# Kernel tuning notes

Measured on AMD Instinct MI355X. Metric: run time of the kernel, lower is better.

Reference implementation:

```python
import jax, jax.numpy as jnp
import numpy as np

N_QUBITS = 10
N_LAYERS = 2
QSVT_DEGREE = 3
DT_RANK = 5  # n_qubits // 2
PI = np.float32(np.pi)

# ---- batched statevector simulation helpers (wire 0 = most significant, as in pennylane default.qubit) ----

def _apply_1q(s, wire, U):
    # s: (batch,) + (2,)*n complex; U: (batch,2,2) or (2,2)
    s = jnp.moveaxis(s, 1 + wire, 1)
    shp = s.shape
    s2 = s.reshape(shp[0], 2, -1)
    if U.ndim == 3:
        out = jnp.einsum('bij,bjr->bir', U, s2)
    else:
        out = jnp.einsum('ij,bjr->bir', U, s2)
    return jnp.moveaxis(out.reshape(shp), 1, 1 + wire)

def _ry(t):
    c = jnp.cos(t / 2).astype(jnp.complex64)
    s = jnp.sin(t / 2).astype(jnp.complex64)
    return jnp.stack([jnp.stack([c, -s], -1), jnp.stack([s, c], -1)], -2)

def _rz(t):
    e = jnp.exp(-0.5j * jnp.asarray(t).astype(jnp.complex64))
    z = jnp.zeros_like(e)
    return jnp.stack([jnp.stack([e, z], -1), jnp.stack([z, jnp.conj(e)], -1)], -2)

def _rx(t):
    c = jnp.cos(t / 2).astype(jnp.complex64)
    s = (-1j) * jnp.sin(t / 2).astype(jnp.complex64)
    return jnp.stack([jnp.stack([c, s], -1), jnp.stack([s, c], -1)], -2)

def _cnot(s, control, target):
    f = jnp.flip(s, axis=1 + target)
    s0 = jax.lax.index_in_dim(s, 0, axis=1 + control, keepdims=True)
    f1 = jax.lax.index_in_dim(f, 1, axis=1 + control, keepdims=True)
    return jnp.concatenate([s0, f1], axis=1 + control)

def _circuit(h, x, dt, cp, pc):
    """Batched selective QSVT circuit; h,x,dt: (B,n). Returns <Z_i> per wire, (B,n) float32."""
    n = N_QUBITS
    b = h.shape[0]
    s = jnp.zeros((b, 2 ** n), jnp.complex64).at[:, 0].set(1.0).reshape((b,) + (2,) * n)
    # 1. state encoding
    for i in range(n):
        s = _apply_1q(s, i, _ry(h[:, i]))
    # 2. delta-modulated QSVT block
    for d in range(QSVT_DEGREE + 1):
        for i in range(n):
            s = _apply_1q(s, i, _rz(pc[d] * dt[:, i] * PI))
        for i in range(n - 1):
            s = _cnot(s, i, i + 1)
        s = _cnot(s, n - 1, 0)
    # 3. variational block
    k = 0
    for _ in range(N_LAYERS):
        for i in range(n):
            s = _apply_1q(s, i, _rx(cp[k]))
            s = _apply_1q(s, i, _ry(cp[k + 1]))
            s = _apply_1q(s, i, _rz(cp[k + 2]))
            k += 3
        for i in range(n - 1):
            s = _cnot(s, i, i + 1)
    # 4. delta-modulated input encoding
    for i in range(n):
        s = _apply_1q(s, i, _ry(x[:, i] * dt[:, i]))
    # 5. <Z_i> measurements
    p = s.real ** 2 + s.imag ** 2
    zs = [(jax.lax.index_in_dim(p, 0, 1 + i, False) - jax.lax.index_in_dim(p, 1, 1 + i, False)).reshape(b, -1).sum(-1) for i in range(n)]
    return jnp.stack(zs, -1).astype(jnp.float32)

def setup_inputs() -> dict:
    key = jax.random.key(0)
    ks = jax.random.split(key, 6)
    B, S, n, r = 128, 512, N_QUBITS, DT_RANK
    angles = jax.random.uniform(ks[0], (B, S, n), jnp.float32) * PI  # angle encoding in [0, pi]
    W_x = jax.random.normal(ks[1], (r + 2 * n, n), jnp.float32) * 0.3  # x_proj weight (no bias)
    W_dt = jax.random.normal(ks[2], (n, r), jnp.float32) * 0.3  # dt_proj weight
    rng = np.random.default_rng(0)
    dt0 = np.exp(rng.random(n) * (np.log(0.1) - np.log(0.001)) + np.log(0.001))
    b_dt = jnp.asarray(dt0 + np.log(-np.expm1(-dt0)), jnp.float32)  # inverse-softplus init
    poly_coeffs = jax.random.normal(ks[3], (QSVT_DEGREE + 1,), jnp.float32) * 0.1
    circuit_params = jax.random.normal(ks[4], (n * N_LAYERS * 3,), jnp.float32) * 0.1
    D = jnp.ones((n,), jnp.float32)
    return {"angles": angles, "W_x": W_x, "W_dt": W_dt, "b_dt": b_dt,
            "poly_coeffs": poly_coeffs, "circuit_params": circuit_params, "D": D}

def reference(angles, W_x, W_dt, b_dt, poly_coeffs, circuit_params, D):
    # selective projections
    x_dbc = jnp.einsum('bsn,kn->bsk', angles, W_x)
    dt_raw = x_dbc[..., :DT_RANK]
    # B slice (x_dbc[..., DT_RANK:DT_RANK+n]) is computed but unused in the original forward
    C = x_dbc[..., DT_RANK + N_QUBITS:]
    dt = jax.nn.softplus(jnp.einsum('bsr,nr->bsn', dt_raw, W_dt) + b_dt)
    dt_angles = jnp.tanh(dt) * PI
    # quantum recurrence uses detached tensors in the original (torch .detach())
    x_sg = jax.lax.stop_gradient(angles)
    dt_sg = jax.lax.stop_gradient(dt_angles)
    cp = jax.lax.stop_gradient(circuit_params)
    pc = jax.lax.stop_gradient(poly_coeffs)

    def step(h, xs):
        x_t, d_t = xs
        h2 = _circuit(h, x_t, d_t, cp, pc)
        return h2, h2

    h0 = jnp.zeros((angles.shape[0], N_QUBITS), jnp.float32)
    _, hs = jax.lax.scan(step, h0, (jnp.swapaxes(x_sg, 0, 1), jnp.swapaxes(dt_sg, 0, 1)))
    hs = jnp.swapaxes(hs, 0, 1)  # (B,S,n)
    return C * hs + D * angles
```

## Files before the change

### kernel.cpp

```cpp
#include <hip/hip_runtime.h>
#include <math.h>


#define PIF 3.14159265358979323846f

constexpr int NQ = 10, SEQ = 512, NB = 128, NTHR = 512;

struct CTbl { int mz[4][NQ]; };
constexpr CTbl build_tbl() {
  CTbl t{};
  unsigned mrow[NQ];
  for (int b = 0; b < NQ; ++b) mrow[b] = 1u << b;
  for (int d = 0; d < 4; ++d) {
    for (int i = 0; i < NQ; ++i) t.mz[d][i] = (int)mrow[9 - i];
    for (int i = 0; i < NQ - 1; ++i) { int bc = 9 - i, bt = 8 - i; mrow[bt] ^= mrow[bc]; }
    mrow[9] ^= mrow[0];
  }
  return t;
}
constexpr CTbl CT = build_tbl();

struct PermCols { int c4[10]; int cL[10]; };
constexpr PermCols build_perms() {
  PermCols P{};
  for (int b = 0; b < 10; ++b) {
    int x = 1 << b;
    for (int d = 0; d < 4; ++d) {
      for (int i = 0; i < 9; ++i) { int bc = 9 - i, bt = 8 - i; if ((x >> bc) & 1) x ^= (1 << bt); }
      if (x & 1) x ^= (1 << 9);
    }
    P.c4[b] = x;
    int y = 1 << b;
    for (int i = 0; i < 9; ++i) { int bc = 9 - i, bt = 8 - i; if ((y >> bc) & 1) y ^= (1 << bt); }
    P.cL[b] = y;
  }
  return P;
}
constexpr PermCols PC = build_perms();

constexpr int lanePart(int x)  { return ((x >> 0) & 1) | (((x >> 5) & 1) << 1) |
                                        (((x >> 1) & 1) << 2) | (((x >> 7) & 1) << 3) |
                                        (((x >> 3) & 1) << 4) | (((x >> 9) & 1) << 5); }
constexpr int wavePart8(int x) { return ((x >> 4) & 1) | (((x >> 8) & 1) << 1) |
                                        (((x >> 6) & 1) << 2); }

constexpr int kmap(int x) {
  return ((x >> 2) & 1)
       | (((x >> 0) & 1) << 1) | (((x >> 5) & 1) << 2) | (((x >> 1) & 1) << 3)
       | (((x >> 7) & 1) << 4) | (((x >> 3) & 1) << 5) | (((x >> 9) & 1) << 6)
       | (((x >> 4) & 1) << 7) | (((x >> 8) & 1) << 8) | (((x >> 6) & 1) << 9);
}
constexpr int swzk(int k) { return k ^ (((k >> 5) & 1) << 1) ^ (((k >> 4) & 1) << 2); }

constexpr int SKC4 = swzk(kmap(PC.c4[2]));
constexpr int SKCL = swzk(kmap(PC.cL[2]));

typedef __attribute__((ext_vector_type(2))) float v2;

template<int C>
__device__ __forceinline__ int dpp1(int x) {
  return __builtin_amdgcn_update_dpp(x, x, C, 0xF, 0xF, false);
}
template<int VL>
__device__ __forceinline__ int lxi(int x) {
  if constexpr (VL == 1)  return dpp1<0xB1>(x);
  else if constexpr (VL == 2)  return dpp1<0x4E>(x);
  else if constexpr (VL == 3)  return dpp1<0x1B>(x);
  else if constexpr (VL <= 7) {
    constexpr int q = (VL & 3) ^ 3;
    int y = x;
    if constexpr (q == 1) y = dpp1<0xB1>(y);
    else if constexpr (q == 2) y = dpp1<0x4E>(y);
    else if constexpr (q == 3) y = dpp1<0x1B>(y);
    return dpp1<0x141>(y);
  } else if constexpr (VL >= 12) {
    constexpr int q = (VL & 3) ^ 3;
    int y = x;
    if constexpr (q == 1) y = dpp1<0xB1>(y);
    else if constexpr (q == 2) y = dpp1<0x4E>(y);
    else if constexpr (q == 3) y = dpp1<0x1B>(y);
    return dpp1<0x140>(y);
  } else {
    constexpr int a = VL & 3;
    int y = x;
    if constexpr (a == 1) y = dpp1<0xB1>(y);
    else if constexpr (a == 2) y = dpp1<0x4E>(y);
    else if constexpr (a == 3) y = dpp1<0x1B>(y);
    y = dpp1<0x141>(y);
    return dpp1<0x140>(y);
  }
}

template<int VL>
__device__ __forceinline__ float2 plpair(float x) {
  int xi = __float_as_int(x);
  if constexpr (VL == 16) {
    auto r = __builtin_amdgcn_permlane16_swap(xi, xi, false, false);
    return make_float2(__int_as_float(r[0]), __int_as_float(r[1]));
  } else {
    static_assert(VL == 32, "plpair supports 16/32 only");
    auto r = __builtin_amdgcn_permlane32_swap(xi, xi, false, false);
    return make_float2(__int_as_float(r[0]), __int_as_float(r[1]));
  }
}
template<int VL>
__device__ __forceinline__ float plsum(float x) {
  float2 p = plpair<VL>(x);
  return p.x + p.y;
}

template<int VL>
__device__ __forceinline__ float lx(float x) {
  if constexpr (VL == 0) return x;
  else if constexpr (VL & 32) {
    int addr = (((int)threadIdx.x & 63) ^ VL) << 2;
    return __int_as_float(__builtin_amdgcn_ds_bpermute(addr, __float_as_int(x)));
  } else if constexpr (VL & 16) {
    return __int_as_float(__builtin_amdgcn_ds_swizzle(__float_as_int(x), (VL << 10) | 0x1F));
  } else {
    return __int_as_float(lxi<VL>(__float_as_int(x)));
  }
}
__device__ __forceinline__ float rdl(float x, int l) {
  return __int_as_float(__builtin_amdgcn_readlane(__float_as_int(x), l));
}

__device__ __forceinline__ void apply2(v2* amp, const v2* p, bool par, float4 U0, float4 U1) {
  v2 u00 = {U0.x, U0.y}, u01 = {U0.z, U0.w}, u10 = {U1.x, U1.y}, u11 = {U1.z, U1.w};
  v2 A = par ? u11 : u00, B = par ? u10 : u01;
  v2 An = {-A.y, A.y}, Bn = {-B.y, B.y};
#pragma unroll
  for (int r = 0; r < 2; ++r) {
    v2 o = amp[r], q = p[r];
    v2 res = A.x * o;
    res += An * __builtin_shufflevector(o, o, 1, 0);
    res += B.x * q;
    res += Bn * __builtin_shufflevector(q, q, 1, 0);
    amp[r] = res;
  }
}

template<int VL>
__device__ __forceinline__ void gate_lane2(v2* amp, float4 U0, float4 U1, int lane) {
  v2 p[2];
#pragma unroll
  for (int r = 0; r < 2; ++r) { p[r].x = lx<VL>(amp[r].x); p[r].y = lx<VL>(amp[r].y); }
  apply2(amp, p, (lane & VL) != 0, U0, U1);
}

__device__ __forceinline__ void gate_reg1(v2* amp, float4 U0, float4 U1) {
  v2 u00 = {U0.x, U0.y}, u01 = {U0.z, U0.w}, u10 = {U1.x, U1.y}, u11 = {U1.z, U1.w};
  v2 o0 = amp[0], o1 = amp[1];
  v2 a0, a1;
  a0.x = u00.x * o0.x - u00.y * o0.y + u01.x * o1.x - u01.y * o1.y;
  a0.y = u00.x * o0.y + u00.y * o0.x + u01.x * o1.y + u01.y * o1.x;
  a1.x = u10.x * o0.x - u10.y * o0.y + u11.x * o1.x - u11.y * o1.y;
  a1.y = u10.x * o0.y + u10.y * o0.x + u11.x * o1.y + u11.y * o1.x;
  amp[0] = a0; amp[1] = a1;
}

template<int VL>
__device__ __forceinline__ float xdot_lane2(const v2* amp) {
  if constexpr (VL == 16 || VL == 32) {
    float acc = 0.f;
#pragma unroll
    for (int r = 0; r < 2; ++r) {
      float2 px = plpair<VL>(amp[r].x);
      float2 py = plpair<VL>(amp[r].y);
      acc += px.x * px.y + py.x * py.y;
    }
    return acc;
  } else {
    v2 acc = {0.f, 0.f};
#pragma unroll
    for (int r = 0; r < 2; ++r) {
      v2 p; p.x = lx<VL>(amp[r].x); p.y = lx<VL>(amp[r].y);
      acc += amp[r] * p;
    }
    return acc.x + acc.y;
  }
}

__global__ __launch_bounds__(NTHR, 2) void qmamba_main(
    const float* __restrict__ angles, const float* __restrict__ Wx,
    const float* __restrict__ Wdt, const float* __restrict__ bdt,
    const float* __restrict__ pc, const float* __restrict__ cp,
    float* __restrict__ out)
{
  __shared__ __align__(16) float tbl[SEQ][30];
  __shared__ float4 uuL[40];
  __shared__ __align__(16) v2 ex0[1024];
  __shared__ __align__(16) v2 ex1[1024];
  __shared__ float  zb[8][16];

  const int tid  = threadIdx.x;
  const int lane = tid & 63;
  const int wv   = tid >> 6;
  const int b    = blockIdx.x;

  if (tid < 20) {
    int k = tid * 3;
    float al = 0.5f * cp[k], be = 0.5f * cp[k + 1], ga = 0.5f * cp[k + 2];
    float ca = __cosf(al), sa = __sinf(al);
    float cb = __cosf(be), sb = __sinf(be);
    float cg = __cosf(ga), sg = __sinf(ga);
    float2 M00 = make_float2(cb * ca,  sb * sa);
    float2 M01 = make_float2(-sb * ca, -cb * sa);
    float2 M10 = make_float2(sb * ca,  -cb * sa);
    float2 M11 = make_float2(cb * ca,  -sb * sa);
    float2 e0 = make_float2(cg, -sg), e1 = make_float2(cg, sg);
    auto cm = [](float2 a, float2 c) {
      return make_float2(a.x * c.x - a.y * c.y, a.x * c.y + a.y * c.x);
    };
    float2 u00 = cm(M00, e0), u01 = cm(M01, e0), u10 = cm(M10, e1), u11 = cm(M11, e1);
    uuL[2 * tid]     = make_float4(u00.x, u00.y, u01.x, u01.y);
    uuL[2 * tid + 1] = make_float4(u10.x, u10.y, u11.x, u11.y);
  }

  {
    const int t = tid;
    const float* ar = angles + (size_t)(b * SEQ + t) * NQ;
    float a[NQ];
#pragma unroll
    for (int n = 0; n < NQ; ++n) a[n] = ar[n];
    float dtr[5];
#pragma unroll
    for (int r = 0; r < 5; ++r) {
      float acc = 0.f;
#pragma unroll
      for (int n = 0; n < NQ; ++n) acc += a[n] * Wx[r * NQ + n];
      dtr[r] = acc;
    }
    float* rec = &tbl[t][0];
#pragma unroll
    for (int w = 0; w < NQ; ++w) {
      float lin = bdt[w];
#pragma unroll
      for (int r = 0; r < 5; ++r) lin += dtr[r] * Wdt[w * 5 + r];
      float sp = lin > 0.f ? lin + log1pf(__expf(-lin)) : log1pf(__expf(lin));
      float th = tanhf(sp) * PIF;
      float fa = a[w] * th;
      rec[w]      = th;
      rec[10 + w] = __cosf(fa);
      rec[20 + w] = __sinf(fa);
    }
  }
  __syncthreads();

  v2 cw0[8], cw1[8];
  {
    const int s5 = wv & 1, s1 = (wv >> 1) & 1, s3 = (wv >> 2) & 1;
    auto ent = [&](int g, int row, int col) -> v2 {
      float4 R = uuL[2 * g + row];
      return col ? v2{R.z, R.w} : v2{R.x, R.y};
    };
    auto cmul = [](v2 a, v2 c) -> v2 {
      return v2{a.x * c.x - a.y * c.y, a.x * c.y + a.y * c.x};
    };
#pragma unroll
    for (int v = 0; v < 8; ++v) {
      const int v5 = v & 1, v1 = (v >> 1) & 1, v3 = (v >> 2) & 1;
      cw0[v] = cmul(cmul(ent(5,  s5, s5 ^ v5), ent(1,  s1, s1 ^ v1)), ent(3,  s3, s3 ^ v3));
      cw1[v] = cmul(cmul(ent(15, s5, s5 ^ v5), ent(11, s1, s1 ^ v1)), ent(13, s3, s3 ^ v3));
    }
  }

  float Kp[NQ], Km[NQ];
  {
    float pch[4];
#pragma unroll
    for (int d = 0; d < 4; ++d) pch[d] = 0.5f * pc[d] * PIF;
#pragma unroll
    for (int i = 0; i < NQ; ++i) {
      float k0 = 0.f, k1 = 0.f;
#pragma unroll
      for (int d = 0; d < 4; ++d) {
        const int m  = CT.mz[d][i];
        const int lm = lanePart(m), wm = wavePart8(m);
        const int rb = (m >> 2) & 1;
        const int p0 = (__popc(lane & lm) ^ __popc(wv & wm)) & 1;
        k0 += p0 ? pch[d] : -pch[d];
        k1 += (p0 ^ rb) ? pch[d] : -pch[d];
      }
      Kp[i] = k0; Km[i] = k1;
    }
  }

  int d4k = 0, dLk = 0;
  if (lane & 1)  { d4k ^= kmap(PC.c4[0]); dLk ^= kmap(PC.cL[0]); }
  if (lane & 2)  { d4k ^= kmap(PC.c4[5]); dLk ^= kmap(PC.cL[5]); }
  if (lane & 4)  { d4k ^= kmap(PC.c4[1]); dLk ^= kmap(PC.cL[1]); }
  if (lane & 8)  { d4k ^= kmap(PC.c4[7]); dLk ^= kmap(PC.cL[7]); }
  if (lane & 16) { d4k ^= kmap(PC.c4[3]); dLk ^= kmap(PC.cL[3]); }
  if (lane & 32) { d4k ^= kmap(PC.c4[9]); dLk ^= kmap(PC.cL[9]); }
  if (wv & 1)    { d4k ^= kmap(PC.c4[4]); dLk ^= kmap(PC.cL[4]); }
  if (wv & 2)    { d4k ^= kmap(PC.c4[8]); dLk ^= kmap(PC.cL[8]); }
  if (wv & 4)    { d4k ^= kmap(PC.c4[6]); dLk ^= kmap(PC.cL[6]); }
  const int sd4  = swzk(d4k);
  const int sdL  = swzk(dLk);
  const int sown = swzk((lane << 1) | (wv << 7));

  float hcw[NQ], hsw[NQ];
#pragma unroll
  for (int w = 0; w < NQ; ++w) { hcw[w] = 1.f; hsw[w] = 0.f; }

  v2 amp[2];

#pragma unroll 1
  for (int t = 0; t < SEQ; ++t) {
    float thv[10];
    {
      const float2* rq = (const float2*)&tbl[t][0];
#pragma unroll
      for (int j = 0; j < 5; ++j) { float2 q = rq[j]; thv[2 * j] = q.x; thv[2 * j + 1] = q.y; }
    }

    float F;
    F  = (lane & 1)  ? hsw[9] : hcw[9];
    F *= (lane & 2)  ? hsw[4] : hcw[4];
    F *= (lane & 4)  ? hsw[8] : hcw[8];
    F *= (lane & 8)  ? hsw[2] : hcw[2];
    F *= (lane & 16) ? hsw[6] : hcw[6];
    F *= (lane & 32) ? hsw[0] : hcw[0];
    F *= (wv & 1)    ? hsw[5] : hcw[5];
    F *= (wv & 2)    ? hsw[1] : hcw[1];
    F *= (wv & 4)    ? hsw[3] : hcw[3];
    const float G0 = F * hcw[7];
    const float G1 = F * hsw[7];

    float Sa = 0.f, Sb = 0.f;
#pragma unroll
    for (int i = 0; i < NQ; ++i) { Sa += Kp[i] * thv[i]; Sb += Km[i] * thv[i]; }
    {
      float sn, cs;
      __sincosf(Sa, &sn, &cs); amp[0].x = G0 * cs; amp[0].y = G0 * sn;
      __sincosf(Sb, &sn, &cs); amp[1].x = G1 * cs; amp[1].y = G1 * sn;
    }

    ex0[sd4]        = amp[0];
    ex0[sd4 ^ SKC4] = amp[1];
    __syncthreads();
    {
      const float4* q4 = (const float4*)ex0;
      v2 a0 = {0.f, 0.f}, a1 = {0.f, 0.f};
#pragma unroll
      for (int v = 0; v < 8; ++v) {
        float4 q = q4[(sown ^ (v << 7)) >> 1];
        v2 c = cw0[v];
        a0.x += c.x * q.x - c.y * q.y;  a0.y += c.x * q.y + c.y * q.x;
        a1.x += c.x * q.z - c.y * q.w;  a1.y += c.x * q.w + c.y * q.z;
      }
      amp[0] = a0; amp[1] = a1;
    }
    gate_lane2<32>(amp, uuL[0],  uuL[1],  lane);
    gate_lane2<8> (amp, uuL[4],  uuL[5],  lane);
    gate_lane2<2> (amp, uuL[8],  uuL[9],  lane);
    gate_lane2<16>(amp, uuL[12], uuL[13], lane);
    gate_reg1     (amp, uuL[14], uuL[15]);
    gate_lane2<4> (amp, uuL[16], uuL[17], lane);
    gate_lane2<1> (amp, uuL[18], uuL[19], lane);

    ex1[sdL]        = amp[0];
    ex1[sdL ^ SKCL] = amp[1];
    __syncthreads();
    {
      const float4* q4 = (const float4*)ex1;
      v2 a0 = {0.f, 0.f}, a1 = {0.f, 0.f};
#pragma unroll
      for (int v = 0; v < 8; ++v) {
        float4 q = q4[(sown ^ (v << 7)) >> 1];
        v2 c = cw1[v];
        a0.x += c.x * q.x - c.y * q.y;  a0.y += c.x * q.y + c.y * q.x;
        a1.x += c.x * q.z - c.y * q.w;  a1.y += c.x * q.w + c.y * q.z;
      }
      amp[0] = a0; amp[1] = a1;
    }
    gate_lane2<32>(amp, uuL[20], uuL[21], lane);
    gate_lane2<8> (amp, uuL[24], uuL[25], lane);
    gate_lane2<2> (amp, uuL[28], uuL[29], lane);
    gate_lane2<16>(amp, uuL[32], uuL[33], lane);
    gate_reg1     (amp, uuL[34], uuL[35]);
    gate_lane2<4> (amp, uuL[36], uuL[37], lane);
    gate_lane2<1> (amp, uuL[38], uuL[39], lane);

    ex0[sdL]        = amp[0];
    ex0[sdL ^ SKCL] = amp[1];
    __syncthreads();
    v2 pw5[2], pw1[2], pw3[2];
    {
      const float4* q4 = (const float4*)ex0;
      float4 qs = q4[sown >> 1];
      float4 q5 = q4[(sown ^ (1 << 7)) >> 1];
      float4 q1 = q4[(sown ^ (2 << 7)) >> 1];
      float4 q3 = q4[(sown ^ (4 << 7)) >> 1];
      amp[0] = v2{qs.x, qs.y}; amp[1] = v2{qs.z, qs.w};
      pw5[0] = v2{q5.x, q5.y}; pw5[1] = v2{q5.z, q5.w};
      pw1[0] = v2{q1.x, q1.y}; pw1[1] = v2{q1.z, q1.w};
      pw3[0] = v2{q3.x, q3.y}; pw3[1] = v2{q3.z, q3.w};
    }

    float cfv[10], sfv[10];
    {
      const float2* rq = (const float2*)&tbl[t][0];
#pragma unroll
      for (int j = 0; j < 5; ++j) {
        float2 qc = rq[5 + j], qsn = rq[10 + j];
        cfv[2 * j] = qc.x; cfv[2 * j + 1] = qc.y;
        sfv[2 * j] = qsn.x; sfv[2 * j + 1] = qsn.y;
      }
    }

    const float n0 = amp[0].x * amp[0].x + amp[0].y * amp[0].y;
    const float n1 = amp[1].x * amp[1].x + amp[1].y * amp[1].y;
    const float T0 = n0 + n1;
    const float T1 = n0 - n1;

    auto vdot2 = [](const v2* a, const v2* p) {
      v2 acc = a[0] * p[0] + a[1] * p[1];
      return acc.x + acc.y;
    };

    float zv[NQ];
    { float zp = (lane & 32) ? -T0 : T0; zv[0] = cfv[0] * zp - sfv[0] * xdot_lane2<32>(amp); }
    { float zp = (wv & 2)    ? -T0 : T0; zv[1] = cfv[1] * zp - sfv[1] * vdot2(amp, pw1); }
    { float zp = (lane & 8)  ? -T0 : T0; zv[2] = cfv[2] * zp - sfv[2] * xdot_lane2<8>(amp); }
    { float zp = (wv & 4)    ? -T0 : T0; zv[3] = cfv[3] * zp - sfv[3] * vdot2(amp, pw3); }
    { float zp = (lane & 2)  ? -T0 : T0; zv[4] = cfv[4] * zp - sfv[4] * xdot_lane2<2>(amp); }
    { float zp = (wv & 1)    ? -T0 : T0; zv[5] = cfv[5] * zp - sfv[5] * vdot2(amp, pw5); }
    { float zp = (lane & 16) ? -T0 : T0; zv[6] = cfv[6] * zp - sfv[6] * xdot_lane2<16>(amp); }
    { float xr = 2.f * (amp[0].x * amp[1].x + amp[0].y * amp[1].y);
      zv[7] = cfv[7] * T1 - sfv[7] * xr; }
    { float zp = (lane & 4)  ? -T0 : T0; zv[8] = cfv[8] * zp - sfv[8] * xdot_lane2<4>(amp); }
    { float zp = (lane & 1)  ? -T0 : T0; zv[9] = cfv[9] * zp - sfv[9] * xdot_lane2<1>(amp); }

#pragma unroll
    for (int w = 0; w < NQ; ++w) {
      zv[w] += lx<1>(zv[w]);
      zv[w] += lx<2>(zv[w]);
      zv[w] += lx<4>(zv[w]);
    }
    const int l7 = lane & 7;
    float c01 = (l7 & 1) ? zv[1] : zv[0];
    float c23 = (l7 & 1) ? zv[3] : zv[2];
    float c45 = (l7 & 1) ? zv[5] : zv[4];
    float c67 = (l7 & 1) ? zv[7] : zv[6];
    float c03 = (l7 & 2) ? c23 : c01;
    float c47 = (l7 & 2) ? c67 : c45;
    float pk  = (l7 & 4) ? c47 : c03;
    pk += lx<8>(pk);  pk = plsum<16>(pk);  pk = plsum<32>(pk);
    float z8 = zv[8]; z8 += lx<8>(z8); z8 = plsum<16>(z8); z8 = plsum<32>(z8);
    float z9 = zv[9]; z9 += lx<8>(z9); z9 = plsum<16>(z9); z9 = plsum<32>(z9);
    float zsel = pk;
    zsel = (lane == 8) ? z8 : zsel;
    zsel = (lane == 9) ? z9 : zsel;

    if (lane < NQ) zb[wv][lane] = zsel;
    __syncthreads();
    float z = 0.f;
    if (lane < NQ) {
      z = zb[0][lane] + zb[1][lane] + zb[2][lane] + zb[3][lane]
        + zb[4][lane] + zb[5][lane] + zb[6][lane] + zb[7][lane];
      if (wv == 0) out[(size_t)(b * SEQ + t) * NQ + lane] = z;
    }
    float sn_h, cs_h;
    __sincosf(0.5f * z, &sn_h, &cs_h);
#pragma unroll
    for (int w = 0; w < NQ; ++w) { hcw[w] = rdl(cs_h, w); hsw[w] = rdl(sn_h, w); }
  }
}

__global__ __launch_bounds__(256) void qmamba_post(
    const float* __restrict__ angles, const float* __restrict__ Wx,
    const float* __restrict__ Dg, float* __restrict__ out)
{
  int i = blockIdx.x * 256 + threadIdx.x;
  if (i >= NB * SEQ * NQ) return;
  int w  = i % NQ;
  int bt = i / NQ;
  const float* a = angles + (size_t)bt * NQ;
  float C = 0.f;
#pragma unroll
  for (int n = 0; n < NQ; ++n) C += a[n] * Wx[(15 + w) * NQ + n];
  float z = out[i];
  out[i] = C * z + Dg[w] * a[w];
}

extern "C" void kernel_launch(void* const* d_in, const int* in_sizes, int n_in,
                              void* d_out, int out_size, void* d_ws, size_t ws_size,
                              hipStream_t stream) {
  (void)in_sizes; (void)n_in; (void)out_size; (void)d_ws; (void)ws_size;
  const float* angles = (const float*)d_in[0];
  const float* Wx     = (const float*)d_in[1];
  const float* Wdt    = (const float*)d_in[2];
  const float* bdt    = (const float*)d_in[3];
  const float* pc     = (const float*)d_in[4];
  const float* cp     = (const float*)d_in[5];
  const float* Dg     = (const float*)d_in[6];
  float* out = (float*)d_out;
  hipLaunchKernelGGL(qmamba_main, dim3(NB), dim3(NTHR), 0, stream,
                     angles, Wx, Wdt, bdt, pc, cp, out);
  hipLaunchKernelGGL(qmamba_post, dim3((NB * SEQ * NQ + 255) / 256), dim3(256), 0, stream,
                     angles, Wx, Dg, out);
}
```

Before: 2.116 ms.

## Process two batch elements per block to amortize barriers and add ILP

Each block now simulates two independent batch recurrences interleaved in the same time loop, halving the grid from 128 to 64 blocks. The two chains share each __syncthreads and the gate-coefficient loads, and their independent instructions can hide latency in the serial per-step dependency chain. The cost is roughly double register and shared-memory use per block (launch bounds drop to one block per CU) and only 64 blocks, so many CUs on the device sit idle.

```diff
diff --git a/kernel.cpp b/kernel.cpp
--- a/kernel.cpp
+++ b/kernel.cpp
@@ -4,7 +4,7 @@
 
 #define PIF 3.14159265358979323846f
 
-constexpr int NQ = 10, SEQ = 512, NB = 128, NTHR = 512;
+constexpr int NQ = 10, SEQ = 512, NBATCH = 128, NTHR = 512, NBLK = 64;
 
 struct CTbl { int mz[4][NQ]; };
 constexpr CTbl build_tbl() {
@@ -181,22 +181,21 @@
   }
 }
 
-__global__ __launch_bounds__(NTHR, 2) void qmamba_main(
+__global__ __launch_bounds__(NTHR, 1) void qmamba_main(
     const float* __restrict__ angles, const float* __restrict__ Wx,
     const float* __restrict__ Wdt, const float* __restrict__ bdt,
     const float* __restrict__ pc, const float* __restrict__ cp,
     float* __restrict__ out)
 {
-  __shared__ __align__(16) float tbl[SEQ][30];
+  __shared__ __align__(16) float tbl[2][SEQ][30];
   __shared__ float4 uuL[40];
-  __shared__ __align__(16) v2 ex0[1024];
-  __shared__ __align__(16) v2 ex1[1024];
-  __shared__ float  zb[8][16];
+  __shared__ __align__(16) v2 ex[2][2][1024];
+  __shared__ float  zb[2][8][16];
 
   const int tid  = threadIdx.x;
   const int lane = tid & 63;
   const int wv   = tid >> 6;
-  const int b    = blockIdx.x;
+  const int b0   = blockIdx.x * 2;
 
   if (tid < 20) {
     int k = tid * 3;
@@ -217,9 +216,10 @@
     uuL[2 * tid + 1] = make_float4(u10.x, u10.y, u11.x, u11.y);
   }
 
-  {
+#pragma unroll 1
+  for (int pel = 0; pel < 2; ++pel) {
     const int t = tid;
-    const float* ar = angles + (size_t)(b * SEQ + t) * NQ;
+    const float* ar = angles + (size_t)((b0 + pel) * SEQ + t) * NQ;
     float a[NQ];
 #pragma unroll
     for (int n = 0; n < NQ; ++n) a[n] = ar[n];
@@ -231,7 +231,7 @@
       for (int n = 0; n < NQ; ++n) acc += a[n] * Wx[r * NQ + n];
       dtr[r] = acc;
     }
-    float* rec = &tbl[t][0];
+    float* rec = &tbl[pel][t][0];
 #pragma unroll
     for (int w = 0; w < NQ; ++w) {
       float lin = bdt[w];
@@ -300,172 +300,282 @@
   const int sdL  = swzk(dLk);
   const int sown = swzk((lane << 1) | (wv << 7));
 
-  float hcw[NQ], hsw[NQ];
-#pragma unroll
-  for (int w = 0; w < NQ; ++w) { hcw[w] = 1.f; hsw[w] = 0.f; }
-
-  v2 amp[2];
+  float hcA[NQ], hsA[NQ], hcB[NQ], hsB[NQ];
+#pragma unroll
+  for (int w = 0; w < NQ; ++w) { hcA[w] = 1.f; hsA[w] = 0.f; hcB[w] = 1.f; hsB[w] = 0.f; }
+
+  v2 ampA[2], ampB[2];
+  v2* const exA0 = &ex[0][0][0];  v2* const exA1 = &ex[0][1][0];
+  v2* const exB0 = &ex[1][0][0];  v2* const exB1 = &ex[1][1][0];
 
 #pragma unroll 1
   for (int t = 0; t < SEQ; ++t) {
-    float thv[10];
-    {
-      const float2* rq = (const float2*)&tbl[t][0];
-#pragma unroll
-      for (int j = 0; j < 5; ++j) { float2 q = rq[j]; thv[2 * j] = q.x; thv[2 * j + 1] = q.y; }
-    }
-
-    float F;
-    F  = (lane & 1)  ? hsw[9] : hcw[9];
-    F *= (lane & 2)  ? hsw[4] : hcw[4];
-    F *= (lane & 4)  ? hsw[8] : hcw[8];
-    F *= (lane & 8)  ? hsw[2] : hcw[2];
-    F *= (lane & 16) ? hsw[6] : hcw[6];
-    F *= (lane & 32) ? hsw[0] : hcw[0];
-    F *= (wv & 1)    ? hsw[5] : hcw[5];
-    F *= (wv & 2)    ? hsw[1] : hcw[1];
-    F *= (wv & 4)    ? hsw[3] : hcw[3];
-    const float G0 = F * hcw[7];
-    const float G1 = F * hsw[7];
-
-    float Sa = 0.f, Sb = 0.f;
-#pragma unroll
-    for (int i = 0; i < NQ; ++i) { Sa += Kp[i] * thv[i]; Sb += Km[i] * thv[i]; }
-    {
+    float thvA[10], thvB[10];
+    {
+      const float2* rqA = (const float2*)&tbl[0][t][0];
+      const float2* rqB = (const float2*)&tbl[1][t][0];
+#pragma unroll
+      for (int j = 0; j < 5; ++j) {
+        float2 qa = rqA[j]; thvA[2 * j] = qa.x; thvA[2 * j + 1] = qa.y;
+        float2 qb = rqB[j]; thvB[2 * j] = qb.x; thvB[2 * j + 1] = qb.y;
+      }
+    }
+
+    {
+      float F;
+      F  = (lane & 1)  ? hsA[9] : hcA[9];
+      F *= (lane & 2)  ? hsA[4] : hcA[4];
+      F *= (lane & 4)  ? hsA[8] : hcA[8];
+      F *= (lane & 8)  ? hsA[2] : hcA[2];
+      F *= (lane & 16) ? hsA[6] : hcA[6];
+      F *= (lane & 32) ? hsA[0] : hcA[0];
+      F *= (wv & 1)    ? hsA[5] : hcA[5];
+      F *= (wv & 2)    ? hsA[1] : hcA[1];
+      F *= (wv & 4)    ? hsA[3] : hcA[3];
+      const float G0 = F * hcA[7], G1 = F * hsA[7];
+      float Sa = 0.f, Sb = 0.f;
+#pragma unroll
+      for (int i = 0; i < NQ; ++i) { Sa += Kp[i] * thvA[i]; Sb += Km[i] * thvA[i]; }
       float sn, cs;
-      __sincosf(Sa, &sn, &cs); amp[0].x = G0 * cs; amp[0].y = G0 * sn;
-      __sincosf(Sb, &sn, &cs); amp[1].x = G1 * cs; amp[1].y = G1 * sn;
-    }
-
-    ex0[sd4]        = amp[0];
-    ex0[sd4 ^ SKC4] = amp[1];
+      __sincosf(Sa, &sn, &cs); ampA[0].x = G0 * cs; ampA[0].y = G0 * sn;
+      __sincosf(Sb, &sn, &cs); ampA[1].x = G1 * cs; ampA[1].y = G1 * sn;
+    }
+    {
+      float F;
+      F  = (lane & 1)  ? hsB[9] : hcB[9];
+      F *= (lane & 2)  ? hsB[4] : hcB[4];
+      F *= (lane & 4)  ? hsB[8] : hcB[8];
+      F *= (lane & 8)  ? hsB[2] : hcB[2];
+      F *= (lane & 16) ? hsB[6] : hcB[6];
+      F *= (lane & 32) ? hsB[0] : hcB[0];
+      F *= (wv & 1)    ? hsB[5] : hcB[5];
+      F *= (wv & 2)    ? hsB[1] : hcB[1];
+      F *= (wv & 4)    ? hsB[3] : hcB[3];
+      const float G0 = F * hcB[7], G1 = F * hsB[7];
+      float Sa = 0.f, Sb = 0.f;
+#pragma unroll
+      for (int i = 0; i < NQ; ++i) { Sa += Kp[i] * thvB[i]; Sb += Km[i] * thvB[i]; }
+      float sn, cs;
+      __sincosf(Sa, &sn, &cs); ampB[0].x = G0 * cs; ampB[0].y = G0 * sn;
+      __sincosf(Sb, &sn, &cs); ampB[1].x = G1 * cs; ampB[1].y = G1 * sn;
+    }
+
+    exA0[sd4]        = ampA[0];
+    exA0[sd4 ^ SKC4] = ampA[1];
+    exB0[sd4]        = ampB[0];
+    exB0[sd4 ^ SKC4] = ampB[1];
     __syncthreads();
     {
-      const float4* q4 = (const float4*)ex0;
-      v2 a0 = {0.f, 0.f}, a1 = {0.f, 0.f};
+      const float4* qA = (const float4*)exA0;
+      const float4* qB = (const float4*)exB0;
+      v2 a0 = {0.f, 0.f}, a1 = {0.f, 0.f}, b0v = {0.f, 0.f}, b1v = {0.f, 0.f};
 #pragma unroll
       for (int v = 0; v < 8; ++v) {
-        float4 q = q4[(sown ^ (v << 7)) >> 1];
+        const int idx = (sown ^ (v << 7)) >> 1;
+        float4 qa = qA[idx];
+        float4 qb = qB[idx];
         v2 c = cw0[v];
-        a0.x += c.x * q.x - c.y * q.y;  a0.y += c.x * q.y + c.y * q.x;
-        a1.x += c.x * q.z - c.y * q.w;  a1.y += c.x * q.w + c.y * q.z;
+        a0.x += c.x * qa.x - c.y * qa.y;  a0.y += c.x * qa.y + c.y * qa.x;
+        a1.x += c.x * qa.z - c.y * qa.w;  a1.y += c.x * qa.w + c.y * qa.z;
+        b0v.x += c.x * qb.x - c.y * qb.y; b0v.y += c.x * qb.y + c.y * qb.x;
+        b1v.x += c.x * qb.z - c.y * qb.w; b1v.y += c.x * qb.w + c.y * qb.z;
       }
-      amp[0] = a0; amp[1] = a1;
-    }
-    gate_lane2<32>(amp, uuL[0],  uuL[1],  lane);
-    gate_lane2<8> (amp, uuL[4],  uuL[5],  lane);
-    gate_lane2<2> (amp, uuL[8],  uuL[9],  lane);
-    gate_lane2<16>(amp, uuL[12], uuL[13], lane);
-    gate_reg1     (amp, uuL[14], uuL[15]);
-    gate_lane2<4> (amp, uuL[16], uuL[17], lane);
-    gate_lane2<1> (amp, uuL[18], uuL[19], lane);
-
-    ex1[sdL]        = amp[0];
-    ex1[sdL ^ SKCL] = amp[1];
+      ampA[0] = a0; ampA[1] = a1; ampB[0] = b0v; ampB[1] = b1v;
+    }
+    gate_lane2<32>(ampA, uuL[0],  uuL[1],  lane);
+    gate_lane2<32>(ampB, uuL[0],  uuL[1],  lane);
+    gate_lane2<8> (ampA, uuL[4],  uuL[5],  lane);
+    gate_lane2<8> (ampB, uuL[4],  uuL[5],  lane);
+    gate_lane2<2> (ampA, uuL[8],  uuL[9],  lane);
+    gate_lane2<2> (ampB, uuL[8],  uuL[9],  lane);
+    gate_lane2<16>(ampA, uuL[12], uuL[13], lane);
+    gate_lane2<16>(ampB, uuL[12], uuL[13], lane);
+    gate_reg1     (ampA, uuL[14], uuL[15]);
+    gate_reg1     (ampB, uuL[14], uuL[15]);
+    gate_lane2<4> (ampA, uuL[16], uuL[17], lane);
+    gate_lane2<4> (ampB, uuL[16], uuL[17], lane);
+    gate_lane2<1> (ampA, uuL[18], uuL[19], lane);
+    gate_lane2<1> (ampB, uuL[18], uuL[19], lane);
+
+    exA1[sdL]        = ampA[0];
+    exA1[sdL ^ SKCL] = ampA[1];
+    exB1[sdL]        = ampB[0];
+    exB1[sdL ^ SKCL] = ampB[1];
     __syncthreads();
     {
-      const float4* q4 = (const float4*)ex1;
-      v2 a0 = {0.f, 0.f}, a1 = {0.f, 0.f};
+      const float4* qA = (const float4*)exA1;
+      const float4* qB = (const float4*)exB1;
+      v2 a0 = {0.f, 0.f}, a1 = {0.f, 0.f}, b0v = {0.f, 0.f}, b1v = {0.f, 0.f};
 #pragma unroll
       for (int v = 0; v < 8; ++v) {
-        float4 q = q4[(sown ^ (v << 7)) >> 1];
+        const int idx = (sown ^ (v << 7)) >> 1;
+        float4 qa = qA[idx];
+        float4 qb = qB[idx];
         v2 c = cw1[v];
-        a0.x += c.x * q.x - c.y * q.y;  a0.y += c.x * q.y + c.y * q.x;
-        a1.x += c.x * q.z - c.y * q.w;  a1.y += c.x * q.w + c.y * q.z;
+        a0.x += c.x * qa.x - c.y * qa.y;  a0.y += c.x * qa.y + c.y * qa.x;
+        a1.x += c.x * qa.z - c.y * qa.w;  a1.y += c.x * qa.w + c.y * qa.z;
+        b0v.x += c.x * qb.x - c.y * qb.y; b0v.y += c.x * qb.y + c.y * qb.x;
+        b1v.x += c.x * qb.z - c.y * qb.w; b1v.y += c.x * qb.w + c.y * qb.z;
       }
-      amp[0] = a0; amp[1] = a1;
-    }
-    gate_lane2<32>(amp, uuL[20], uuL[21], lane);
-    gate_lane2<8> (amp, uuL[24], uuL[25], lane);
-    gate_lane2<2> (amp, uuL[28], uuL[29], lane);
-    gate_lane2<16>(amp, uuL[32], uuL[33], lane);
-    gate_reg1     (amp, uuL[34], uuL[35]);
-    gate_lane2<4> (amp, uuL[36], uuL[37], lane);
-    gate_lane2<1> (amp, uuL[38], uuL[39], lane);
-
-    ex0[sdL]        = amp[0];
-    ex0[sdL ^ SKCL] = amp[1];
+      ampA[0] = a0; ampA[1] = a1; ampB[0] = b0v; ampB[1] = b1v;
+    }
+    gate_lane2<32>(ampA, uuL[20], uuL[21], lane);
+    gate_lane2<32>(ampB, uuL[20], uuL[21], lane);
+    gate_lane2<8> (ampA, uuL[24], uuL[25], lane);
+    gate_lane2<8> (ampB, uuL[24], uuL[25], lane);
+    gate_lane2<2> (ampA, uuL[28], uuL[29], lane);
+    gate_lane2<2> (ampB, uuL[28], uuL[29], lane);
+    gate_lane2<16>(ampA, uuL[32], uuL[33], lane);
+    gate_lane2<16>(ampB, uuL[32], uuL[33], lane);
+    gate_reg1     (ampA, uuL[34], uuL[35]);
+    gate_reg1     (ampB, uuL[34], uuL[35]);
+    gate_lane2<4> (ampA, uuL[36], uuL[37], lane);
+    gate_lane2<4> (ampB, uuL[36], uuL[37], lane);
+    gate_lane2<1> (ampA, uuL[38], uuL[39], lane);
+    gate_lane2<1> (ampB, uuL[38], uuL[39], lane);
+
+    exA0[sdL]        = ampA[0];
+    exA0[sdL ^ SKCL] = ampA[1];
+    exB0[sdL]        = ampB[0];
+    exB0[sdL ^ SKCL] = ampB[1];
     __syncthreads();
-    v2 pw5[2], pw1[2], pw3[2];
-    {
-      const float4* q4 = (const float4*)ex0;
-      float4 qs = q4[sown >> 1];
-      float4 q5 = q4[(sown ^ (1 << 7)) >> 1];
-      float4 q1 = q4[(sown ^ (2 << 7)) >> 1];
-      float4 q3 = q4[(sown ^ (4 << 7)) >> 1];
-      amp[0] = v2{qs.x, qs.y}; amp[1] = v2{qs.z, qs.w};
-      pw5[0] = v2{q5.x, q5.y}; pw5[1] = v2{q5.z, q5.w};
-      pw1[0] = v2{q1.x, q1.y}; pw1[1] = v2{q1.z, q1.w};
-      pw3[0] = v2{q3.x, q3.y}; pw3[1] = v2{q3.z, q3.w};
-    }
-
-    float cfv[10], sfv[10];
-    {
-      const float2* rq = (const float2*)&tbl[t][0];
+    v2 pwA5[2], pwA1[2], pwA3[2], pwB5[2], pwB1[2], pwB3[2];
+    {
+      const float4* qA = (const float4*)exA0;
+      const float4* qB = (const float4*)exB0;
+      float4 qs = qA[sown >> 1];
+      float4 q5 = qA[(sown ^ (1 << 7)) >> 1];
+      float4 q1 = qA[(sown ^ (2 << 7)) >> 1];
+      float4 q3 = qA[(sown ^ (4 << 7)) >> 1];
+      ampA[0] = v2{qs.x, qs.y}; ampA[1] = v2{qs.z, qs.w};
+      pwA5[0] = v2{q5.x, q5.y}; pwA5[1] = v2{q5.z, q5.w};
+      pwA1[0] = v2{q1.x, q1.y}; pwA1[1] = v2{q1.z, q1.w};
+      pwA3[0] = v2{q3.x, q3.y}; pwA3[1] = v2{q3.z, q3.w};
+      qs = qB[sown >> 1];
+      q5 = qB[(sown ^ (1 << 7)) >> 1];
+      q1 = qB[(sown ^ (2 << 7)) >> 1];
+      q3 = qB[(sown ^ (4 << 7)) >> 1];
+      ampB[0] = v2{qs.x, qs.y}; ampB[1] = v2{qs.z, qs.w};
+      pwB5[0] = v2{q5.x, q5.y}; pwB5[1] = v2{q5.z, q5.w};
+      pwB1[0] = v2{q1.x, q1.y}; pwB1[1] = v2{q1.z, q1.w};
+      pwB3[0] = v2{q3.x, q3.y}; pwB3[1] = v2{q3.z, q3.w};
+    }
+
+    auto vdot2 = [](const v2* a, const v2* p) {
+      v2 acc = a[0] * p[0] + a[1] * p[1];
+      return acc.x + acc.y;
+    };
+
+    float zvA[NQ], zvB[NQ];
+    {
+      float cfv[10], sfv[10];
+      const float2* rq = (const float2*)&tbl[0][t][0];
 #pragma unroll
       for (int j = 0; j < 5; ++j) {
         float2 qc = rq[5 + j], qsn = rq[10 + j];
         cfv[2 * j] = qc.x; cfv[2 * j + 1] = qc.y;
         sfv[2 * j] = qsn.x; sfv[2 * j + 1] = qsn.y;
       }
-    }
-
-    const float n0 = amp[0].x * amp[0].x + amp[0].y * amp[0].y;
-    const float n1 = amp[1].x * amp[1].x + amp[1].y * amp[1].y;
-    const float T0 = n0 + n1;
-    const float T1 = n0 - n1;
-
-    auto vdot2 = [](const v2* a, const v2* p) {
-      v2 acc = a[0] * p[0] + a[1] * p[1];
-      return acc.x + acc.y;
-    };
-
-    float zv[NQ];
-    { float zp = (lane & 32) ? -T0 : T0; zv[0] = cfv[0] * zp - sfv[0] * xdot_lane2<32>(amp); }
-    { float zp = (wv & 2)    ? -T0 : T0; zv[1] = cfv[1] * zp - sfv[1] * vdot2(amp, pw1); }
-    { float zp = (lane & 8)  ? -T0 : T0; zv[2] = cfv[2] * zp - sfv[2] * xdot_lane2<8>(amp); }
-    { float zp = (wv & 4)    ? -T0 : T0; zv[3] = cfv[3] * zp - sfv[3] * vdot2(amp, pw3); }
-    { float zp = (lane & 2)  ? -T0 : T0; zv[4] = cfv[4] * zp - sfv[4] * xdot_lane2<2>(amp); }
-    { float zp = (wv & 1)    ? -T0 : T0; zv[5] = cfv[5] * zp - sfv[5] * vdot2(amp, pw5); }
-    { float zp = (lane & 16) ? -T0 : T0; zv[6] = cfv[6] * zp - sfv[6] * xdot_lane2<16>(amp); }
-    { float xr = 2.f * (amp[0].x * amp[1].x + amp[0].y * amp[1].y);
-      zv[7] = cfv[7] * T1 - sfv[7] * xr; }
-    { float zp = (lane & 4)  ? -T0 : T0; zv[8] = cfv[8] * zp - sfv[8] * xdot_lane2<4>(amp); }
-    { float zp = (lane & 1)  ? -T0 : T0; zv[9] = cfv[9] * zp - sfv[9] * xdot_lane2<1>(amp); }
+      const float n0 = ampA[0].x * ampA[0].x + ampA[0].y * ampA[0].y;
+      const float n1 = ampA[1].x * ampA[1].x + ampA[1].y * ampA[1].y;
+      const float T0 = n0 + n1, T1 = n0 - n1;
+      { float zp = (lane & 32) ? -T0 : T0; zvA[0] = cfv[0] * zp - sfv[0] * xdot_lane2<32>(ampA); }
+      { float zp = (wv & 2)    ? -T0 : T0; zvA[1] = cfv[1] * zp - sfv[1] * vdot2(ampA, pwA1); }
+      { float zp = (lane & 8)  ? -T0 : T0; zvA[2] = cfv[2] * zp - sfv[2] * xdot_lane2<8>(ampA); }
+      { float zp = (wv & 4)    ? -T0 : T0; zvA[3] = cfv[3] * zp - sfv[3] * vdot2(ampA, pwA3); }
+      { float zp = (lane & 2)  ? -T0 : T0; zvA[4] = cfv[4] * zp - sfv[4] * xdot_lane2<2>(ampA); }
+      { float zp = (wv & 1)    ? -T0 : T0; zvA[5] = cfv[5] * zp - sfv[5] * vdot2(ampA, pwA5); }
+      { float zp = (lane & 16) ? -T0 : T0; zvA[6] = cfv[6] * zp - sfv[6] * xdot_lane2<16>(ampA); }
+      { float xr = 2.f * (ampA[0].x * ampA[1].x + ampA[0].y * ampA[1].y);
+        zvA[7] = cfv[7] * T1 - sfv[7] * xr; }
+      { float zp = (lane & 4)  ? -T0 : T0; zvA[8] = cfv[8] * zp - sfv[8] * xdot_lane2<4>(ampA); }
+      { float zp = (lane & 1)  ? -T0 : T0; zvA[9] = cfv[9] * zp - sfv[9] * xdot_lane2<1>(ampA); }
+    }
+    {
+      float cfv[10], sfv[10];
+      const float2* rq = (const float2*)&tbl[1][t][0];
+#pragma unroll
+      for (int j = 0; j < 5; ++j) {
+        float2 qc = rq[5 + j], qsn = rq[10 + j];
+        cfv[2 * j] = qc.x; cfv[2 * j + 1] = qc.y;
+        sfv[2 * j] = qsn.x; sfv[2 * j + 1] = qsn.y;
+      }
+      const float n0 = ampB[0].x * ampB[0].x + ampB[0].y * ampB[0].y;
+      const float n1 = ampB[1].x * ampB[1].x + ampB[1].y * ampB[1].y;
+      const float T0 = n0 + n1, T1 = n0 - n1;
+      { float zp = (lane & 32) ? -T0 : T0; zvB[0] = cfv[0] * zp - sfv[0] * xdot_lane2<32>(ampB); }
+      { float zp = (wv & 2)    ? -T0 : T0; zvB[1] = cfv[1] * zp - sfv[1] * vdot2(ampB, pwB1); }
+      { float zp = (lane & 8)  ? -T0 : T0; zvB[2] = cfv[2] * zp - sfv[2] * xdot_lane2<8>(ampB); }
+      { float zp = (wv & 4)    ? -T0 : T0; zvB[3] = cfv[3] * zp - sfv[3] * vdot2(ampB, pwB3); }
+      { float zp = (lane & 2)  ? -T0 : T0; zvB[4] = cfv[4] * zp - sfv[4] * xdot_lane2<2>(ampB); }
+      { float zp = (wv & 1)    ? -T0 : T0; zvB[5] = cfv[5] * zp - sfv[5] * vdot2(ampB, pwB5); }
+      { float zp = (lane & 16) ? -T0 : T0; zvB[6] = cfv[6] * zp - sfv[6] * xdot_lane2<16>(ampB); }
+      { float xr = 2.f * (ampB[0].x * ampB[1].x + ampB[0].y * ampB[1].y);
+        zvB[7] = cfv[7] * T1 - sfv[7] * xr; }
+      { float zp = (lane & 4)  ? -T0 : T0; zvB[8] = cfv[8] * zp - sfv[8] * xdot_lane2<4>(ampB); }
+      { float zp = (lane & 1)  ? -T0 : T0; zvB[9] = cfv[9] * zp - sfv[9] * xdot_lane2<1>(ampB); }
+    }
 
 #pragma unroll
     for (int w = 0; w < NQ; ++w) {
-      zv[w] += lx<1>(zv[w]);
-      zv[w] += lx<2>(zv[w]);
-      zv[w] += lx<4>(zv[w]);
+      zvA[w] += lx<1>(zvA[w]);  zvB[w] += lx<1>(zvB[w]);
+      zvA[w] += lx<2>(zvA[w]);  zvB[w] += lx<2>(zvB[w]);
+      zvA[w] += lx<4>(zvA[w]);  zvB[w] += lx<4>(zvB[w]);
     }
     const int l7 = lane & 7;
-    float c01 = (l7 & 1) ? zv[1] : zv[0];
-    float c23 = (l7 & 1) ? zv[3] : zv[2];
-    float c45 = (l7 & 1) ? zv[5] : zv[4];
-    float c67 = (l7 & 1) ? zv[7] : zv[6];
-    float c03 = (l7 & 2) ? c23 : c01;
-    float c47 = (l7 & 2) ? c67 : c45;
-    float pk  = (l7 & 4) ? c47 : c03;
-    pk += lx<8>(pk);  pk = plsum<16>(pk);  pk = plsum<32>(pk);
-    float z8 = zv[8]; z8 += lx<8>(z8); z8 = plsum<16>(z8); z8 = plsum<32>(z8);
-    float z9 = zv[9]; z9 += lx<8>(z9); z9 = plsum<16>(z9); z9 = plsum<32>(z9);
-    float zsel = pk;
-    zsel = (lane == 8) ? z8 : zsel;
-    zsel = (lane == 9) ? z9 : zsel;
-
-    if (lane < NQ) zb[wv][lane] = zsel;
+    float zselA, zselB;
+    {
+      float c01 = (l7 & 1) ? zvA[1] : zvA[0];
+      float c23 = (l7 & 1) ? zvA[3] : zvA[2];
+      float c45 = (l7 & 1) ? zvA[5] : zvA[4];
+      float c67 = (l7 & 1) ? zvA[7] : zvA[6];
+      float c03 = (l7 & 2) ? c23 : c01;
+      float c47 = (l7 & 2) ? c67 : c45;
+      float pk  = (l7 & 4) ? c47 : c03;
+      pk += lx<8>(pk);  pk = plsum<16>(pk);  pk = plsum<32>(pk);
+      float z8 = zvA[8]; z8 += lx<8>(z8); z8 = plsum<16>(z8); z8 = plsum<32>(z8);
+      float z9 = zvA[9]; z9 += lx<8>(z9); z9 = plsum<16>(z9); z9 = plsum<32>(z9);
+      zselA = pk;
+      zselA = (lane == 8) ? z8 : zselA;
+      zselA = (lane == 9) ? z9 : zselA;
+    }
+    {
+      float c01 = (l7 & 1) ? zvB[1] : zvB[0];
+      float c23 = (l7 & 1) ? zvB[3] : zvB[2];
+      float c45 = (l7 & 1) ? zvB[5] : zvB[4];
+      float c67 = (l7 & 1) ? zvB[7] : zvB[6];
+      float c03 = (l7 & 2) ? c23 : c01;
+      float c47 = (l7 & 2) ? c67 : c45;
+      float pk  = (l7 & 4) ? c47 : c03;
+      pk += lx<8>(pk);  pk = plsum<16>(pk);  pk = plsum<32>(pk);
+      float z8 = zvB[8]; z8 += lx<8>(z8); z8 = plsum<16>(z8); z8 = plsum<32>(z8);
+      float z9 = zvB[9]; z9 += lx<8>(z9); z9 = plsum<16>(z9); z9 = plsum<32>(z9);
+      zselB = pk;
+      zselB = (lane == 8) ? z8 : zselB;
+      zselB = (lane == 9) ? z9 : zselB;
+    }
+
+    if (lane < NQ) { zb[0][wv][lane] = zselA; zb[1][wv][lane] = zselB; }
     __syncthreads();
-    float z = 0.f;
+    float zA = 0.f, zB = 0.f;
     if (lane < NQ) {
-      z = zb[0][lane] + zb[1][lane] + zb[2][lane] + zb[3][lane]
-        + zb[4][lane] + zb[5][lane] + zb[6][lane] + zb[7][lane];
-      if (wv == 0) out[(size_t)(b * SEQ + t) * NQ + lane] = z;
-    }
-    float sn_h, cs_h;
-    __sincosf(0.5f * z, &sn_h, &cs_h);
-#pragma unroll
-    for (int w = 0; w < NQ; ++w) { hcw[w] = rdl(cs_h, w); hsw[w] = rdl(sn_h, w); }
+      zA = zb[0][0][lane] + zb[0][1][lane] + zb[0][2][lane] + zb[0][3][lane]
+         + zb[0][4][lane] + zb[0][5][lane] + zb[0][6][lane] + zb[0][7][lane];
+      zB = zb[1][0][lane] + zb[1][1][lane] + zb[1][2][lane] + zb[1][3][lane]
+         + zb[1][4][lane] + zb[1][5][lane] + zb[1][6][lane] + zb[1][7][lane];
+      if (wv == 0) {
+        out[(size_t)(b0 * SEQ + t) * NQ + lane]       = zA;
+        out[(size_t)((b0 + 1) * SEQ + t) * NQ + lane] = zB;
+      }
+    }
+    float snA, csA, snB, csB;
+    __sincosf(0.5f * zA, &snA, &csA);
+    __sincosf(0.5f * zB, &snB, &csB);
+#pragma unroll
+    for (int w = 0; w < NQ; ++w) {
+      hcA[w] = rdl(csA, w); hsA[w] = rdl(snA, w);
+      hcB[w] = rdl(csB, w); hsB[w] = rdl(snB, w);
+    }
   }
 }
 
@@ -474,7 +584,7 @@
     const float* __restrict__ Dg, float* __restrict__ out)
 {
   int i = blockIdx.x * 256 + threadIdx.x;
-  if (i >= NB * SEQ * NQ) return;
+  if (i >= NBATCH * SEQ * NQ) return;
   int w  = i % NQ;
   int bt = i / NQ;
   const float* a = angles + (size_t)bt * NQ;
@@ -497,8 +607,8 @@
   const float* cp     = (const float*)d_in[5];
   const float* Dg     = (const float*)d_in[6];
   float* out = (float*)d_out;
-  hipLaunchKernelGGL(qmamba_main, dim3(NB), dim3(NTHR), 0, stream,
+  hipLaunchKernelGGL(qmamba_main, dim3(NBLK), dim3(NTHR), 0, stream,
                      angles, Wx, Wdt, bdt, pc, cp, out);
-  hipLaunchKernelGGL(qmamba_post, dim3((NB * SEQ * NQ + 255) / 256), dim3(256), 0, stream,
+  hipLaunchKernelGGL(qmamba_post, dim3((NBATCH * SEQ * NQ + 255) / 256), dim3(256), 0, stream,
                      angles, Wx, Dg, out);
 }
```

After: 3.674 ms. 1.74x slower.
